# Performance work log

Measured on AMD Instinct MI355X. Metric: run time of the kernel, lower is better.

The kernel has to match this reference:

```python
import jax, jax.numpy as jnp
import numpy as np

B, N, T, IN_DIM, OUT_DIM = 16, 500, 12, 2, 2
H, D, K, NH, NBLOCKS, T_OUT, GDEP = 64, 64, 10, 24, 2, 12, 2
H2 = 2 * H


def setup_inputs():
    key = jax.random.key(0)
    ks = iter(jax.random.split(key, 64))

    def rn(shape, s=1.0):
        return jax.random.normal(next(ks), shape, dtype=jnp.float32) * s

    def z(*shape):
        return jnp.zeros(shape, jnp.float32)

    sI = 1.0 / np.sqrt(IN_DIM)
    sH = 1.0 / np.sqrt(H)
    sH2 = 1.0 / np.sqrt(H2)
    sD = 1.0 / np.sqrt(D)
    adj = jax.random.uniform(next(ks), (N, N), dtype=jnp.float32)
    inp = {
        'x': rn((B, N, T, IN_DIM)),
        'weather': rn((B, T, 4)),
        'geo_adj': adj / adj.sum(1, keepdims=True),
        'fcx_W': rn((IN_DIM, H), sI), 'fcx_b': z(H),
        'env_cb': rn((K, D)), 'nodes_cb': rn((N, D)),
        'w_v': rn((D, K), sD), 'w_k': rn((D, D), sD), 'w_q': rn((D, D), sD),
        'core_W': rn((H, H * H), sH), 'core_b': z(H * H),
        'tcnN_Win': rn((K, H2, H2), sH2), 'tcnN_bin': z(K, H2),
        'tcnN_Wf': rn((K, NBLOCKS, 2, H2, H2), sH2), 'tcnN_bf': z(K, NBLOCKS, H2),
        'tcnN_Wg': rn((K, NBLOCKS, 2, H2, H2), sH2), 'tcnN_bg': z(K, NBLOCKS, H2),
        'tcnN_Wout': rn((K, H2, H), sH2), 'tcnN_bout': z(K, H),
        'tcnP_Win': rn((K, H2, H2), sH2), 'tcnP_bin': z(K, H2),
        'tcnP_Wf': rn((K, NBLOCKS, 2, H2, H2), sH2), 'tcnP_bf': z(K, NBLOCKS, H2),
        'tcnP_Wg': rn((K, NBLOCKS, 2, H2, H2), sH2), 'tcnP_bg': z(K, NBLOCKS, H2),
        'tcnP_Wout': rn((K, H2, H), sH2), 'tcnP_bout': z(K, H),
        'bn1_g': jnp.ones((H,), jnp.float32), 'bn1_b': z(H),
        'bnP_g': jnp.ones((H,), jnp.float32), 'bnP_b': z(H),
        'gcn1_W': rn((H, H), sH), 'gcn1_b': z(H),
        'gcn2_W': rn((H, H), sH), 'gcn2_b': z(H),
        'gcnp_W': rn((H, H), sH), 'gcnp_b': z(H),
        'nv_p1': rn((2 * NH, H)), 'nv_p2': rn((N, H)), 'nv_p3': rn((N, H)),
        'nv_pk': rn((H, H, H), sH),
        'out_W1': rn((T_OUT, H, 100), sH), 'out_b1': z(T_OUT, 100),
        'out_W2': rn((T_OUT, 100, OUT_DIM), 0.1), 'out_b2': z(T_OUT, OUT_DIM),
        't_pos': jax.random.randint(next(ks), (B, T, 2), 0, 7),
        'ind': jax.random.randint(next(ks), (B, T, 2), 0, 7),
    }
    return inp


def _tstep_emb(t, dim):
    half = dim // 2
    freqs = jnp.exp(-jnp.log(10000.0) * jnp.arange(half, dtype=jnp.float32) / half)
    a = t.astype(jnp.float32)[:, None] * freqs[None]
    return jnp.concatenate([jnp.cos(a), jnp.sin(a)], -1)


def _conv2(h, W, b, d):
    # causal kernel-2 dilated conv over time: h [B,N,T,C], W [2,C,Co] -> [B,N,T-d,Co]
    return (jnp.einsum('bntc,co->bnto', h[:, :, :-d], W[0])
            + jnp.einsum('bntc,co->bnto', h[:, :, d:], W[1]) + b)


def _tcn(xin, Win, bin_, Wf, bf, Wg, bg, Wout, bout):
    # gated dilated TCN (Graph-WaveNet style), per node over time
    h = jnp.einsum('bntc,co->bnto', xin, Win) + bin_
    for l in range(Wf.shape[0]):
        d = 2 ** l
        f = jnp.tanh(_conv2(h, Wf[l], bf[l], d))
        g = jax.nn.sigmoid(_conv2(h, Wg[l], bg[l], d))
        h = f * g + h[:, :, d:, :]
    return jnp.einsum('bntc,ch->bnth', h, Wout) + bout


def _bn(h, g, b):
    # BatchNorm1d over channels, stats over (batch, nodes); training mode
    mu = h.mean((0, 1))
    var = h.var((0, 1))
    return g * (h - mu) * jax.lax.rsqrt(var + 1e-5) + b


def _gcn(h, adj, W, b):
    # multi-hop diffusion: sum_{k=0..GDEP} A^k h, then linear
    eq = 'nm,bmh->bnh' if adj.ndim == 2 else 'bnm,bmh->bnh'
    acc, zt = h, h
    for _ in range(GDEP):
        zt = jnp.einsum(eq, adj, zt)
        acc = acc + zt
    return jnp.einsum('bnh,ho->bno', acc, W) + b


def _forward(x, weather, geo_adj, fcx_W, fcx_b, env_cb, nodes_cb, w_v, w_k, w_q,
             core_W, core_b,
             tcnN_Win, tcnN_bin, tcnN_Wf, tcnN_bf, tcnN_Wg, tcnN_bg, tcnN_Wout, tcnN_bout,
             tcnP_Win, tcnP_bin, tcnP_Wf, tcnP_bf, tcnP_Wg, tcnP_bg, tcnP_Wout, tcnP_bout,
             bn1_g, bn1_b, bnP_g, bnP_b, gcn1_W, gcn1_b, gcn2_W, gcn2_b, gcnp_W, gcnp_b,
             nv_p1, nv_p2, nv_p3, nv_pk, out_W1, out_b1, out_W2, out_b2, t_pos, ind):
    scale = 1.0 / jnp.sqrt(jnp.float32(D))
    ind_p = jnp.where(ind[:, :, 0] <= 4, ind[:, :, 1], NH - 1 + ind[:, :, 1])
    tp = jnp.where(t_pos[:, :, 0] <= 4, t_pos[:, :, 1], NH - 1 + t_pos[:, :, 1])
    t_emb = _tstep_emb(tp.reshape(-1), H).reshape(B, T, H)

    # codebook attention -> hard cluster assignment (gumbel softmax, straight-through)
    mat_v = env_cb @ w_v
    mat_k = env_cb @ w_k
    mat_q = nodes_cb @ w_q
    scores = jax.nn.softmax((mat_q @ mat_k.T) * scale, axis=1)
    logits = scores @ mat_v                                   # [N,K]
    gn = jax.random.gumbel(jax.random.key(42), logits.shape, dtype=logits.dtype)
    y_soft = jax.nn.softmax(logits + gn, axis=1)
    hard = jax.nn.one_hot(jnp.argmax(y_soft, axis=1), K, dtype=y_soft.dtype)
    mask = y_soft + jax.lax.stop_gradient(hard - y_soft)      # [N,K] one-hot fwd

    x_emb = jnp.einsum('bnti,ih->bnth', x, fcx_W) + fcx_b
    total_x = jnp.concatenate(
        [x_emb, jnp.broadcast_to(t_emb[:, None], (B, N, T, H))], -1)  # [B,N,T,2H]

    unbias = jnp.zeros((B, N, H), total_x.dtype)
    h_prev = jnp.zeros((B, N, H), total_x.dtype)
    for i in range(K):  # small fixed cluster count
        m = mask[:, i]
        xm = total_x * m[None, :, None, None]
        hn = _tcn(xm[:, :, 1:], tcnN_Win[i], tcnN_bin[i], tcnN_Wf[i], tcnN_bf[i],
                  tcnN_Wg[i], tcnN_bg[i], tcnN_Wout[i], tcnN_bout[i])[:, :, 0, :]
        hp = _tcn(xm[:, :, :-1], tcnP_Win[i], tcnP_bin[i], tcnP_Wf[i], tcnP_bf[i],
                  tcnP_Wg[i], tcnP_bg[i], tcnP_Wout[i], tcnP_bout[i])[:, :, 0, :]
        unbias = unbias + m[None, :, None] * hn
        h_prev = h_prev + m[None, :, None] * hp

    unbias = _bn(unbias, bn1_g, bn1_b)
    h_prev = _bn(h_prev, bnP_g, bnP_b)

    h1 = _gcn(h_prev, geo_adj, gcn1_W, gcn1_b)
    core = (t_emb[:, T - 1] @ core_W + core_b).reshape(B, H, H)
    causal = jax.nn.softmax(jnp.einsum('bnh,bhk,bmk->bnm', unbias, core, h_prev), axis=-1)
    h2 = _gcn(unbias, causal, gcn2_W, gcn2_b)

    te = nv_p1[ind_p[:, -(T - 1)]]                            # [B,H]
    adp = jnp.einsum('ai,ijk->ajk', te, nv_pk)
    adp = jnp.einsum('bj,ajk->abk', nv_p2, adp)
    adp = jnp.einsum('ck,abk->abc', nv_p3, adp)
    adp = jax.nn.softmax(jax.nn.relu(adp), axis=2)            # [B,N,N]
    h3 = _gcn(unbias, adp, gcnp_W, gcnp_b)

    cur_h = h1 + h2 + h3
    hmid = jax.nn.elu(jnp.einsum('bnh,thf->bntf', cur_h, out_W1) + out_b1)
    return jnp.einsum('bntf,tfo->bnto', hmid, out_W2) + out_b2  # [B,N,T_OUT,OUT_DIM]


def reference(x, weather, geo_adj, fcx_W, fcx_b, env_cb, nodes_cb, w_v, w_k, w_q,
              core_W, core_b,
              tcnN_Win, tcnN_bin, tcnN_Wf, tcnN_bf, tcnN_Wg, tcnN_bg, tcnN_Wout, tcnN_bout,
              tcnP_Win, tcnP_bin, tcnP_Wf, tcnP_bf, tcnP_Wg, tcnP_bg, tcnP_Wout, tcnP_bout,
              bn1_g, bn1_b, bnP_g, bnP_b, gcn1_W, gcn1_b, gcn2_W, gcn2_b, gcnp_W, gcnp_b,
              nv_p1, nv_p2, nv_p3, nv_pk, out_W1, out_b1, out_W2, out_b2, t_pos, ind):
    return _forward(x, weather, geo_adj, fcx_W, fcx_b, env_cb, nodes_cb, w_v, w_k, w_q,
                    core_W, core_b,
                    tcnN_Win, tcnN_bin, tcnN_Wf, tcnN_bf, tcnN_Wg, tcnN_bg, tcnN_Wout, tcnN_bout,
                    tcnP_Win, tcnP_bin, tcnP_Wf, tcnP_bf, tcnP_Wg, tcnP_bg, tcnP_Wout, tcnP_bout,
                    bn1_g, bn1_b, bnP_g, bnP_b, gcn1_W, gcn1_b, gcn2_W, gcn2_b, gcnp_W, gcnp_b,
                    nv_p1, nv_p2, nv_p3, nv_pk, out_W1, out_b1, out_W2, out_b2, t_pos, ind)
```

## Files before the change

kernel.cpp:

```cpp
#include <hip/hip_runtime.h>
#include <hip/hip_bf16.h>
#include <math.h>

#define B_ 16
#define N_ 500
#define T_ 12
#define K_ 10
#define NROWS (B_*N_)
#define TROWS 6

__device__ __forceinline__ unsigned rotl32(unsigned v, int r){ return (v<<r)|(v>>(32-r)); }

__device__ __forceinline__ void threefry2x32(unsigned k0, unsigned k1,
                                             unsigned c0, unsigned c1,
                                             unsigned &o0, unsigned &o1){
  unsigned ks2 = k0 ^ k1 ^ 0x1BD11BDAu;
  unsigned x0 = c0 + k0, x1 = c1 + k1;
#define TF_R(r) { x0 += x1; x1 = rotl32(x1,(r)); x1 ^= x0; }
  TF_R(13) TF_R(15) TF_R(26) TF_R(6)
  x0 += k1;  x1 += ks2 + 1u;
  TF_R(17) TF_R(29) TF_R(16) TF_R(24)
  x0 += ks2; x1 += k0 + 2u;
  TF_R(13) TF_R(15) TF_R(26) TF_R(6)
  x0 += k0;  x1 += k1 + 3u;
  TF_R(17) TF_R(29) TF_R(16) TF_R(24)
  x0 += k1;  x1 += ks2 + 4u;
  TF_R(13) TF_R(15) TF_R(26) TF_R(6)
  x0 += ks2; x1 += k0 + 5u;
#undef TF_R
  o0 = x0; o1 = x1;
}

__device__ __forceinline__ float gumbel_at(unsigned idx){
  unsigned b0, b1;
  threefry2x32(0u, 42u, 0u, idx, b0, b1);
  unsigned bits = b0 ^ b1;
  float u = __uint_as_float((bits >> 9) | 0x3f800000u) - 1.0f;
  u = fmaxf(u, 1.17549435e-38f);
  return -logf(-logf(u));
}

__global__ __launch_bounds__(256) void k_matq(const float* __restrict__ nodes_cb,
                                              const float* __restrict__ w_q,
                                              float* __restrict__ matq){
  int idx = blockIdx.x*256 + threadIdx.x;
  if (idx >= N_*64) return;
  int n = idx >> 6, d = idx & 63;
  float a = 0.f;
  for (int c = 0; c < 64; ++c) a += nodes_cb[n*64+c] * w_q[c*64+d];
  matq[idx] = a;
}

__global__ __launch_bounds__(256) void k_route(const float* __restrict__ env_cb,
                                               const float* __restrict__ w_v,
                                               const float* __restrict__ w_k,
                                               const float* __restrict__ matq,
                                               int* __restrict__ node_list,
                                               int* __restrict__ off){
  __shared__ float smk[K_*64];
  __shared__ float smv[K_*K_];
  __shared__ int sroute[N_];
  int tid = threadIdx.x;
  for (int idx = tid; idx < K_*64; idx += 256){
    int kk = idx >> 6, d = idx & 63;
    float a = 0.f;
    for (int c = 0; c < 64; ++c) a += env_cb[kk*64+c] * w_k[c*64+d];
    smk[idx] = a;
  }
  for (int idx = tid; idx < K_*K_; idx += 256){
    int kk = idx / K_, j = idx % K_;
    float a = 0.f;
    for (int c = 0; c < 64; ++c) a += env_cb[kk*64+c] * w_v[c*K_+j];
    smv[idx] = a;
  }
  __syncthreads();
  for (int n = tid; n < N_; n += 256){
    float s[K_];
    float mx = -1e30f;
    for (int j = 0; j < K_; ++j){
      float a = 0.f;
      for (int d = 0; d < 64; ++d) a += matq[n*64+d]*smk[j*64+d];
      s[j] = a * 0.125f;
      mx = fmaxf(mx, s[j]);
    }
    float sum = 0.f;
    for (int j = 0; j < K_; ++j){ s[j] = expf(s[j]-mx); sum += s[j]; }
    float inv = 1.f/sum;
    int best = 0; float bestv = -1e30f;
    for (int j2 = 0; j2 < K_; ++j2){
      float lg = 0.f;
      for (int j = 0; j < K_; ++j) lg += s[j]*inv*smv[j*K_+j2];
      float tot = lg + gumbel_at((unsigned)(n*K_+j2));
      if (tot > bestv){ bestv = tot; best = j2; }
    }
    sroute[n] = best;
  }
  __syncthreads();
  if (tid == 0){
    int cnt[K_]; for (int j=0;j<K_;++j) cnt[j]=0;
    for (int n=0;n<N_;++n) cnt[sroute[n]]++;
    int acc=0;
    for (int j=0;j<K_;++j){ off[j]=acc; acc+=cnt[j]; }
    off[K_]=acc;
    int pos[K_]; for (int j=0;j<K_;++j) pos[j]=off[j];
    for (int n=0;n<N_;++n) node_list[pos[sroute[n]]++] = n;
  }
}

__global__ void k_temb(const int* __restrict__ t_pos, float* __restrict__ temb){
  int tid = threadIdx.x;
  if (tid >= B_*T_) return;
  int b = tid / T_, t = tid % T_;
  int p0 = t_pos[(b*T_+t)*2+0], p1 = t_pos[(b*T_+t)*2+1];
  float tp = (float)((p0 <= 4) ? p1 : 23 + p1);
  float c0 = -logf(10000.f)/32.f;
  for (int j = 0; j < 32; ++j){
    float a = tp * expf(c0 * (float)j);
    temb[(b*T_+t)*64 + j]      = cosf(a);
    temb[(b*T_+t)*64 + 32 + j] = sinf(a);
  }
}

__global__ __launch_bounds__(256) void k_core(const float* __restrict__ temb,
                                              const float* __restrict__ core_W,
                                              const float* __restrict__ core_b,
                                              float* __restrict__ core_f){
  int idx = blockIdx.x*256 + threadIdx.x;
  if (idx >= B_*4096) return;
  int b = idx >> 12, c = idx & 4095;
  const float* te = temb + (b*T_ + 11)*64;
  float a = core_b[c];
  for (int h = 0; h < 64; ++h) a += te[h] * core_W[h*4096 + c];
  core_f[idx] = a;
}

__global__ __launch_bounds__(256) void k_tmp1(const int* __restrict__ ind,
                                              const float* __restrict__ nv_p1,
                                              const float* __restrict__ nv_pk,
                                              float* __restrict__ tmp1){
  int idx = blockIdx.x*256 + threadIdx.x;
  if (idx >= B_*4096) return;
  int b = idx >> 12, c = idx & 4095;
  int i0 = ind[(b*T_+1)*2+0], i1 = ind[(b*T_+1)*2+1];
  int row = (i0 <= 4) ? i1 : 23 + i1;
  const float* te = nv_p1 + row*64;
  float a = 0.f;
  for (int h = 0; h < 64; ++h) a += te[h] * nv_pk[h*4096 + c];
  tmp1[idx] = a;
}

__global__ __launch_bounds__(128) void k_tprep(
    const float* __restrict__ temb,
    const float* __restrict__ fcx_W, const float* __restrict__ fcx_b,
    const float* __restrict__ WinN, const float* __restrict__ WinP,
    float* __restrict__ TE)
{
  int slot = blockIdx.x;
  int y = blockIdx.y;
  int k = slot >> 1, path = slot & 1;
  const float* Win = (path ? WinP : WinN) + k*16384;
  int o = threadIdx.x;
  if (y < 80){
    __shared__ float ste[64];
    int b = y/5, t = y%5;
    if (o < 64) ste[o] = temb[(b*T_ + t)*64 + o];
    __syncthreads();
    float acc = 0.f;
    for (int cc = 0; cc < 64; ++cc) acc += ste[cc] * Win[(64+cc)*128 + o];
    TE[slot*10240 + y*128 + o] = acc;
  } else {
    float a0=0.f, a1=0.f, c0=0.f;
    for (int c = 0; c < 64; ++c){
      float w = Win[c*128 + o];
      a0 += fcx_W[c]*w; a1 += fcx_W[64+c]*w; c0 += fcx_b[c]*w;
    }
    float* AAs = TE + 20*10240 + slot*384;
    AAs[o] = a0; AAs[128+o] = a1; AAs[256+o] = c0;
  }
}

__global__ __launch_bounds__(256) void k_tcn2(
    const float* __restrict__ x,
    const float* __restrict__ TE,
    const int* __restrict__ node_list, const int* __restrict__ off,
    const float* __restrict__ binN,
    const float* __restrict__ WfN,  const float* __restrict__ bfN,
    const float* __restrict__ WgN,  const float* __restrict__ bgN,
    const float* __restrict__ WoutN,const float* __restrict__ boutN,
    const float* __restrict__ binP,
    const float* __restrict__ WfP,  const float* __restrict__ bfP,
    const float* __restrict__ WgP,  const float* __restrict__ bgP,
    const float* __restrict__ WoutP,const float* __restrict__ boutP,
    float* __restrict__ out_unb, float* __restrict__ out_hpr)
{
  int slot = blockIdx.x;
  int k = slot >> 1;
  int path = slot & 1;
  int cnt = off[k+1] - off[k];
  int rows = cnt * 16;
  int r0 = blockIdx.y * TROWS;
  if (r0 >= rows) return;

  const float* bin  = (path ? binP  : binN)  + k*128;
  const float* Wf   = (path ? WfP   : WfN)   + k*4*16384;
  const float* bf_  = (path ? bfP   : bfN)   + k*2*128;
  const float* Wg   = (path ? WgP   : WgN)   + k*4*16384;
  const float* bg_  = (path ? bgP   : bgN)   + k*2*128;
  const float* Wout = (path ? WoutP : WoutN) + k*8192;
  const float* bout = (path ? boutP : boutN) + k*64;
  float* outb = path ? out_hpr : out_unb;
  int t0 = path ? 0 : 1;

  __shared__ __align__(16) float sH0[TROWS*512];
  __shared__ __align__(16) float sH1[TROWS*256];
  __shared__ __align__(16) float sH2[TROWS*128];
  __shared__ float xs[TROWS][4][2];
  __shared__ int rowBN[TROWS];
  __shared__ int rowB[TROWS];

  int tid = threadIdx.x;
  if (tid < TROWS){
    int r = r0 + tid;
    if (r < rows){
      int node = node_list[off[k] + (r >> 4)];
      int b = r & 15;
      rowBN[tid] = b*N_ + node;
      rowB[tid]  = b;
    } else { rowBN[tid] = -1; rowB[tid] = 0; }
  }
  __syncthreads();
  if (tid < TROWS*4){
    int i = tid >> 2, tl = tid & 3;
    int rb = rowBN[i];
    float x0 = 0.f, x1 = 0.f;
    if (rb >= 0){
      const float* xp = x + (rb*T_ + tl + t0)*2;
      x0 = xp[0]; x1 = xp[1];
    }
    xs[i][tl][0] = x0; xs[i][tl][1] = x1;
  }
  __syncthreads();

  {
    int o = tid & 127, half = tid >> 7;
    const float* AAs = TE + 20*10240 + slot*384;
    const float* TEs = TE + slot*10240;
    float a0 = AAs[o], a1 = AAs[128+o], c0 = AAs[256+o];
    float bn = bin[o];
    #pragma unroll
    for (int jj = 0; jj < 12; ++jj){
      int rt = half*12 + jj;
      int i = rt >> 2, tl = rt & 3;
      float v = xs[i][tl][0]*a0 + xs[i][tl][1]*a1 + c0
              + TEs[(rowB[i]*5 + tl + t0)*128 + o] + bn;
      sH0[rt*128 + o] = v;
    }
  }
  __syncthreads();

  {
    int o = tid & 127;
    int jg = (tid >> 7)*6;
    float af[6], ag[6];
    #pragma unroll
    for (int j=0;j<6;++j){ af[j]=0.f; ag[j]=0.f; }
    for (int c = 0; c < 128; c += 4){
      float f00=Wf[(c+0)*128+o], f01=Wf[(c+1)*128+o], f02=Wf[(c+2)*128+o], f03=Wf[(c+3)*128+o];
      float f10=Wf[16384+(c+0)*128+o], f11=Wf[16384+(c+1)*128+o], f12=Wf[16384+(c+2)*128+o], f13=Wf[16384+(c+3)*128+o];
      float g00=Wg[(c+0)*128+o], g01=Wg[(c+1)*128+o], g02=Wg[(c+2)*128+o], g03=Wg[(c+3)*128+o];
      float g10=Wg[16384+(c+0)*128+o], g11=Wg[16384+(c+1)*128+o], g12=Wg[16384+(c+2)*128+o], g13=Wg[16384+(c+3)*128+o];
      #pragma unroll
      for (int jj=0;jj<6;++jj){
        int j = jg + jj;
        int i = j >> 1, ti = j & 1;
        float4 xa = *(const float4*)&sH0[(i*4+ti*2  )*128 + c];
        float4 xb = *(const float4*)&sH0[(i*4+ti*2+1)*128 + c];
        af[jj] += xa.x*f00 + xa.y*f01 + xa.z*f02 + xa.w*f03
                + xb.x*f10 + xb.y*f11 + xb.z*f12 + xb.w*f13;
        ag[jj] += xa.x*g00 + xa.y*g01 + xa.z*g02 + xa.w*g03
                + xb.x*g10 + xb.y*g11 + xb.z*g12 + xb.w*g13;
      }
    }
    float bfv = bf_[o], bgv = bg_[o];
    #pragma unroll
    for (int jj=0;jj<6;++jj){
      int j = jg + jj;
      int i = j >> 1, ti = j & 1;
      float f = tanhf(af[jj] + bfv);
      float g = 1.f/(1.f + expf(-(ag[jj] + bgv)));
      sH1[j*128 + o] = f*g + sH0[(i*4 + ti*2 + 1)*128 + o];
    }
  }
  __syncthreads();

  {
    int o = tid & 127;
    int ig = (tid >> 7)*3;
    const float* Wf1 = Wf + 2*16384;
    const float* Wg1 = Wg + 2*16384;
    float af[3], ag[3];
    #pragma unroll
    for (int i=0;i<3;++i){ af[i]=0.f; ag[i]=0.f; }
    for (int c = 0; c < 128; c += 4){
      float f00=Wf1[(c+0)*128+o], f01=Wf1[(c+1)*128+o], f02=Wf1[(c+2)*128+o], f03=Wf1[(c+3)*128+o];
      float f10=Wf1[16384+(c+0)*128+o], f11=Wf1[16384+(c+1)*128+o], f12=Wf1[16384+(c+2)*128+o], f13=Wf1[16384+(c+3)*128+o];
      float g00=Wg1[(c+0)*128+o], g01=Wg1[(c+1)*128+o], g02=Wg1[(c+2)*128+o], g03=Wg1[(c+3)*128+o];
      float g10=Wg1[16384+(c+0)*128+o], g11=Wg1[16384+(c+1)*128+o], g12=Wg1[16384+(c+2)*128+o], g13=Wg1[16384+(c+3)*128+o];
      #pragma unroll
      for (int ii=0;ii<3;++ii){
        int i = ig + ii;
        float4 xa = *(const float4*)&sH1[(i*2+0)*128 + c];
        float4 xb = *(const float4*)&sH1[(i*2+1)*128 + c];
        af[ii] += xa.x*f00 + xa.y*f01 + xa.z*f02 + xa.w*f03
                + xb.x*f10 + xb.y*f11 + xb.z*f12 + xb.w*f13;
        ag[ii] += xa.x*g00 + xa.y*g01 + xa.z*g02 + xa.w*g03
                + xb.x*g10 + xb.y*g11 + xb.z*g12 + xb.w*g13;
      }
    }
    float bfv = bf_[128+o], bgv = bg_[128+o];
    #pragma unroll
    for (int ii=0;ii<3;++ii){
      int i = ig + ii;
      float f = tanhf(af[ii] + bfv);
      float g = 1.f/(1.f + expf(-(ag[ii] + bgv)));
      sH2[i*128 + o] = f*g + sH1[(i*2+1)*128 + o];
    }
  }
  __syncthreads();

  {
    int o6 = tid & 63, grp = tid >> 6;
    #pragma unroll
    for (int ii=0; ii<2; ++ii){
      int i = grp*2 + ii;
      if (i >= TROWS) continue;
      float acc = 0.f;
      for (int c = 0; c < 128; c += 4){
        float w0=Wout[(c+0)*64+o6], w1=Wout[(c+1)*64+o6],
              w2=Wout[(c+2)*64+o6], w3=Wout[(c+3)*64+o6];
        float4 xv = *(const float4*)&sH2[i*128 + c];
        acc += xv.x*w0 + xv.y*w1 + xv.z*w2 + xv.w*w3;
      }
      if (rowBN[i] >= 0) outb[rowBN[i]*64 + o6] = acc + bout[o6];
    }
  }
}

__global__ __launch_bounds__(256) void k_tcn(
    const float* __restrict__ x,
    const float* __restrict__ fcx_W, const float* __restrict__ fcx_b,
    const float* __restrict__ temb,
    const int* __restrict__ node_list, const int* __restrict__ off,
    const float* __restrict__ WinN, const float* __restrict__ binN,
    const float* __restrict__ WfN,  const float* __restrict__ bfN,
    const float* __restrict__ WgN,  const float* __restrict__ bgN,
    const float* __restrict__ WoutN,const float* __restrict__ boutN,
    const float* __restrict__ WinP, const float* __restrict__ binP,
    const float* __restrict__ WfP,  const float* __restrict__ bfP,
    const float* __restrict__ WgP,  const float* __restrict__ bgP,
    const float* __restrict__ WoutP,const float* __restrict__ boutP,
    float* __restrict__ out_unb, float* __restrict__ out_hpr)
{
  int slot = blockIdx.x;
  int k = slot >> 1;
  int path = slot & 1;
  int cnt = off[k+1] - off[k];
  int rows = cnt * 16;
  int r0 = blockIdx.y * TROWS;
  if (r0 >= rows) return;

  const float* Win  = (path ? WinP  : WinN)  + k*16384;
  const float* bin  = (path ? binP  : binN)  + k*128;
  const float* Wf   = (path ? WfP   : WfN)   + k*4*16384;
  const float* bf_  = (path ? bfP   : bfN)   + k*2*128;
  const float* Wg   = (path ? WgP   : WgN)   + k*4*16384;
  const float* bg_  = (path ? bgP   : bgN)   + k*2*128;
  const float* Wout = (path ? WoutP : WoutN) + k*8192;
  const float* bout = (path ? boutP : boutN) + k*64;
  float* outb = path ? out_hpr : out_unb;
  int t0 = path ? 0 : 1;

  __shared__ __align__(16) float sIn[TROWS*512];
  __shared__ __align__(16) float sH0[TROWS*512];
  __shared__ __align__(16) float sH1[TROWS*256];
  __shared__ __align__(16) float sH2[TROWS*128];
  __shared__ int rowBN[TROWS];
  __shared__ int rowB[TROWS];

  int tid = threadIdx.x;
  if (tid < TROWS){
    int r = r0 + tid;
    if (r < rows){
      int node = node_list[off[k] + (r >> 4)];
      int b = r & 15;
      rowBN[tid] = b*N_ + node;
      rowB[tid]  = b;
    } else { rowBN[tid] = -1; rowB[tid] = 0; }
  }
  __syncthreads();

  for (int i = 0; i < TROWS; ++i){
    int rb = rowBN[i], b = rowB[i];
    for (int c2 = tid; c2 < 512; c2 += 256){
      int t = (c2 >> 7) + t0, c = c2 & 127;
      float v = 0.f;
      if (rb >= 0){
        if (c < 64){
          const float* xp = x + (rb*T_ + t)*2;
          v = xp[0]*fcx_W[c] + xp[1]*fcx_W[64+c] + fcx_b[c];
        } else {
          v = temb[(b*T_ + t)*64 + (c-64)];
        }
      }
      sIn[i*512 + c2] = v;
    }
  }
  __syncthreads();

  {
    int oc = (tid & 63)*2;
    int jg = (tid >> 6)*6;
    float a0[6], a1[6];
    #pragma unroll
    for (int j=0;j<6;++j){ a0[j]=0.f; a1[j]=0.f; }
    for (int c = 0; c < 128; c += 4){
      float2 w0 = *(const float2*)(Win + (c+0)*128 + oc);
      float2 w1 = *(const float2*)(Win + (c+1)*128 + oc);
      float2 w2 = *(const float2*)(Win + (c+2)*128 + oc);
      float2 w3 = *(const float2*)(Win + (c+3)*128 + oc);
      #pragma unroll
      for (int j=0;j<6;++j){
        float4 xv = *(const float4*)&sIn[(jg+j)*128 + c];
        a0[j] += xv.x*w0.x + xv.y*w1.x + xv.z*w2.x + xv.w*w3.x;
        a1[j] += xv.x*w0.y + xv.y*w1.y + xv.z*w2.y + xv.w*w3.y;
      }
    }
    float b0v = bin[oc], b1v = bin[oc+1];
    #pragma unroll
    for (int j=0;j<6;++j){
      sH0[(jg+j)*128 + oc]   = a0[j] + b0v;
      sH0[(jg+j)*128 + oc+1] = a1[j] + b1v;
    }
  }
  __syncthreads();

  {
    int o = tid & 127;
    int jg = (tid >> 7)*6;
    float af[6], ag[6];
    #pragma unroll
    for (int j=0;j<6;++j){ af[j]=0.f; ag[j]=0.f; }
    for (int c = 0; c < 128; c += 4){
      float f00=Wf[(c+0)*128+o], f01=Wf[(c+1)*128+o], f02=Wf[(c+2)*128+o], f03=Wf[(c+3)*128+o];
      float f10=Wf[16384+(c+0)*128+o], f11=Wf[16384+(c+1)*128+o], f12=Wf[16384+(c+2)*128+o], f13=Wf[16384+(c+3)*128+o];
      float g00=Wg[(c+0)*128+o], g01=Wg[(c+1)*128+o], g02=Wg[(c+2)*128+o], g03=Wg[(c+3)*128+o];
      float g10=Wg[16384+(c+0)*128+o], g11=Wg[16384+(c+1)*128+o], g12=Wg[16384+(c+2)*128+o], g13=Wg[16384+(c+3)*128+o];
      #pragma unroll
      for (int jj=0;jj<6;++jj){
        int j = jg + jj;
        int i = j >> 1, ti = j & 1;
        float4 xa = *(const float4*)&sH0[(i*4+ti*2  )*128 + c];
        float4 xb = *(const float4*)&sH0[(i*4+ti*2+1)*128 + c];
        af[jj] += xa.x*f00 + xa.y*f01 + xa.z*f02 + xa.w*f03
                + xb.x*f10 + xb.y*f11 + xb.z*f12 + xb.w*f13;
        ag[jj] += xa.x*g00 + xa.y*g01 + xa.z*g02 + xa.w*g03
                + xb.x*g10 + xb.y*g11 + xb.z*g12 + xb.w*g13;
      }
    }
    float bfv = bf_[o], bgv = bg_[o];
    #pragma unroll
    for (int jj=0;jj<6;++jj){
      int j = jg + jj;
      int i = j >> 1, ti = j & 1;
      float f = tanhf(af[jj] + bfv);
      float g = 1.f/(1.f + expf(-(ag[jj] + bgv)));
      sH1[j*128 + o] = f*g + sH0[(i*4 + ti*2 + 1)*128 + o];
    }
  }
  __syncthreads();

  {
    int o = tid & 127;
    int ig = (tid >> 7)*3;
    const float* Wf1 = Wf + 2*16384;
    const float* Wg1 = Wg + 2*16384;
    float af[3], ag[3];
    #pragma unroll
    for (int i=0;i<3;++i){ af[i]=0.f; ag[i]=0.f; }
    for (int c = 0; c < 128; c += 4){
      float f00=Wf1[(c+0)*128+o], f01=Wf1[(c+1)*128+o], f02=Wf1[(c+2)*128+o], f03=Wf1[(c+3)*128+o];
      float f10=Wf1[16384+(c+0)*128+o], f11=Wf1[16384+(c+1)*128+o], f12=Wf1[16384+(c+2)*128+o], f13=Wf1[16384+(c+3)*128+o];
      float g00=Wg1[(c+0)*128+o], g01=Wg1[(c+1)*128+o], g02=Wg1[(c+2)*128+o], g03=Wg1[(c+3)*128+o];
      float g10=Wg1[16384+(c+0)*128+o], g11=Wg1[16384+(c+1)*128+o], g12=Wg1[16384+(c+2)*128+o], g13=Wg1[16384+(c+3)*128+o];
      #pragma unroll
      for (int ii=0;ii<3;++ii){
        int i = ig + ii;
        float4 xa = *(const float4*)&sH1[(i*2+0)*128 + c];
        float4 xb = *(const float4*)&sH1[(i*2+1)*128 + c];
        af[ii] += xa.x*f00 + xa.y*f01 + xa.z*f02 + xa.w*f03
                + xb.x*f10 + xb.y*f11 + xb.z*f12 + xb.w*f13;
        ag[ii] += xa.x*g00 + xa.y*g01 + xa.z*g02 + xa.w*g03
                + xb.x*g10 + xb.y*g11 + xb.z*g12 + xb.w*g13;
      }
    }
    float bfv = bf_[128+o], bgv = bg_[128+o];
    #pragma unroll
    for (int ii=0;ii<3;++ii){
      int i = ig + ii;
      float f = tanhf(af[ii] + bfv);
      float g = 1.f/(1.f + expf(-(ag[ii] + bgv)));
      sH2[i*128 + o] = f*g + sH1[(i*2+1)*128 + o];
    }
  }
  __syncthreads();

  {
    int o6 = tid & 63, grp = tid >> 6;
    #pragma unroll
    for (int ii=0; ii<2; ++ii){
      int i = grp*2 + ii;
      if (i >= TROWS) continue;
      float acc = 0.f;
      for (int c = 0; c < 128; c += 4){
        float w0=Wout[(c+0)*64+o6], w1=Wout[(c+1)*64+o6],
              w2=Wout[(c+2)*64+o6], w3=Wout[(c+3)*64+o6];
        float4 xv = *(const float4*)&sH2[i*128 + c];
        acc += xv.x*w0 + xv.y*w1 + xv.z*w2 + xv.w*w3;
      }
      if (rowBN[i] >= 0) outb[rowBN[i]*64 + o6] = acc + bout[o6];
    }
  }
}

__global__ __launch_bounds__(256) void k_bnstats(const float* __restrict__ unb,
                                                 const float* __restrict__ hpr,
                                                 float* __restrict__ stats){
  int bid = blockIdx.x;
  int tensor = bid >> 6, c = bid & 63;
  const float* buf = tensor ? hpr : unb;
  float s1 = 0.f, s2 = 0.f;
  for (int r = threadIdx.x; r < NROWS; r += 256){
    float v = buf[r*64 + c];
    s1 += v; s2 += v*v;
  }
  __shared__ float r1[256], r2[256];
  r1[threadIdx.x]=s1; r2[threadIdx.x]=s2;
  __syncthreads();
  for (int s=128; s>0; s>>=1){
    if (threadIdx.x < s){ r1[threadIdx.x]+=r1[threadIdx.x+s]; r2[threadIdx.x]+=r2[threadIdx.x+s]; }
    __syncthreads();
  }
  if (threadIdx.x==0){
    float mean = r1[0]/(float)NROWS;
    float var  = r2[0]/(float)NROWS - mean*mean;
    stats[tensor*128 + c]      = mean;
    stats[tensor*128 + 64 + c] = rsqrtf(var + 1e-5f);
  }
}

__global__ __launch_bounds__(256) void k_bnapply(float* __restrict__ unb, float* __restrict__ hpr,
                                                 const float* __restrict__ stats,
                                                 const float* __restrict__ g1, const float* __restrict__ be1,
                                                 const float* __restrict__ gP, const float* __restrict__ beP){
  int idx = blockIdx.x*256 + threadIdx.x;
  if (idx >= 2*NROWS*64) return;
  int tensor = idx >= NROWS*64;
  int local = idx - tensor*NROWS*64;
  int c = local & 63;
  float* buf = tensor ? hpr : unb;
  float mean = stats[tensor*128+c], rstd = stats[tensor*128+64+c];
  float g = tensor ? gP[c] : g1[c];
  float bb = tensor ? beP[c] : be1[c];
  buf[local] = g * (buf[local]-mean) * rstd + bb;
}

template<int AMODE, int RELU, int FINAL, int ADD>
__global__ __launch_bounds__(256) void k_attn(
    const float* __restrict__ geo,
    const float* __restrict__ Qf, const float* __restrict__ Qb,
    const float* __restrict__ M,
    const float* __restrict__ Keysf, const float* __restrict__ Keysb,
    const float* __restrict__ X,
    const float* __restrict__ X0, const float* __restrict__ Z1,
    const float* __restrict__ Wg, const float* __restrict__ bg,
    float* __restrict__ cur, float* __restrict__ Y)
{
  __shared__ __align__(16) float kbuf[64][65];
  __shared__ __align__(16) float xbuf[64][64];
  __shared__ __align__(16) float vbuf[16][64];
  __shared__ __align__(16) float pbuf[16][64];

  int b = blockIdx.y, n0 = blockIdx.x*16;
  int tid = threadIdx.x;
  int nl = tid >> 5, ml = tid & 31;
  int nA = n0 + nl, nB = n0 + nl + 8;
  float rrK[16], rrX[16], rrA[4];

  if (AMODE != 0){
    for (int idx = tid; idx < 1024; idx += 256){
      int r = idx >> 6, kk = idx & 63;
      int nn = n0 + r;
      float q = 0.f;
      if (nn < N_) q = (AMODE == 1) ? Qf[(b*N_+nn)*64+kk] : Qb[nn*64+kk];
      pbuf[r][kk] = q;
    }
    for (int idx = tid; idx < 4096; idx += 256)
      kbuf[idx>>6][idx&63] = M[b*4096 + idx];
    __syncthreads();
    float vxA = 0.f, vyA = 0.f, vxB = 0.f, vyB = 0.f;
    for (int kk = 0; kk < 64; ++kk){
      float qA = pbuf[nl][kk], qB = pbuf[nl+8][kk];
      float2 m2 = *(const float2*)&kbuf[kk][ml*2];
      vxA += qA*m2.x; vyA += qA*m2.y;
      vxB += qB*m2.x; vyB += qB*m2.y;
    }
    __syncthreads();
    vbuf[nl  ][ml*2] = vxA; vbuf[nl  ][ml*2+1] = vyA;
    vbuf[nl+8][ml*2] = vxB; vbuf[nl+8][ml*2+1] = vyB;
  }
  {
    if (AMODE != 0) __syncthreads();
    #pragma unroll
    for (int ii = 0; ii < 16; ++ii){
      int idx = tid + ii*256;
      int mm = idx >> 6, kk = idx & 63;
      if (AMODE != 0)
        kbuf[mm][kk] = (AMODE == 1) ? Keysf[(b*N_+mm)*64+kk] : Keysb[mm*64+kk];
      xbuf[mm][kk] = X[(b*N_+mm)*64+kk];
    }
    if (AMODE == 0){
      #pragma unroll
      for (int ii = 0; ii < 4; ++ii){
        int idx = tid + ii*256;
        int r = idx >> 6, mm = idx & 63;
        int nn = n0 + r;
        pbuf[r][mm] = (nn < N_) ? geo[nn*N_ + mm] : 0.f;
      }
    }
// ... 278 lines not shown
      l_runB = l_runB*scaleB + lcB; m_runB = mnewB;
      accxA *= scaleA; accyA *= scaleA;
      accxB *= scaleB; accyB *= scaleB;
      pbuf[nl  ][ml]    = p0A;
      pbuf[nl  ][ml+32] = p1A;
      pbuf[nl+8][ml]    = p0B;
      pbuf[nl+8][ml+32] = p1B;
    }
    __syncthreads();
    for (int mm = 0; mm < 64; mm += 4){
      float4 pA = *(const float4*)&pbuf[nl  ][mm];
      float4 pB = *(const float4*)&pbuf[nl+8][mm];
      float2 x0 = *(const float2*)&xbuf[mm+0][ml*2];
      float2 x1 = *(const float2*)&xbuf[mm+1][ml*2];
      float2 x2 = *(const float2*)&xbuf[mm+2][ml*2];
      float2 x3 = *(const float2*)&xbuf[mm+3][ml*2];
      accxA += pA.x*x0.x + pA.y*x1.x + pA.z*x2.x + pA.w*x3.x;
      accyA += pA.x*x0.y + pA.y*x1.y + pA.z*x2.y + pA.w*x3.y;
      accxB += pB.x*x0.x + pB.y*x1.x + pB.z*x2.x + pB.w*x3.x;
      accyB += pB.x*x0.y + pB.y*x1.y + pB.z*x2.y + pB.w*x3.y;
    }
    __syncthreads();
    if (ci < 7){
      #pragma unroll
      for (int ii=0; ii<16; ++ii){
        int idx = tid + ii*256;
        kbuf[idx>>6][idx&63] = rrK[ii];
        xbuf[idx>>6][idx&63] = rrX[ii];
      }
      __syncthreads();
    }
  }
  float invA = 1.f / l_runA, invB = 1.f / l_runB;
  accxA *= invA; accyA *= invA;
  accxB *= invB; accyB *= invB;
  if (nA < N_){
    float2 o2; o2.x = accxA; o2.y = accyA;
    *(float2*)&Y[(b*N_+nA)*64 + ml*2] = o2;
  }
  if (nB < N_){
    float2 o2; o2.x = accxB; o2.y = accyB;
    *(float2*)&Y[(b*N_+nB)*64 + ml*2] = o2;
  }
}

template<int ADD>
__global__ __launch_bounds__(256) void k_attn_p2(
    const float* __restrict__ Pb,
    const float* __restrict__ X,
    const float* __restrict__ X0,
    const float* __restrict__ Wg, const float* __restrict__ bg,
    float* __restrict__ cur)
{
  __shared__ __align__(16) float pbuf[16][516];
  __shared__ __align__(16) float xbuf[64][64];
  __shared__ __align__(16) float vbuf[16][64];

  int b = blockIdx.y, n0 = blockIdx.x*16;
  int tid = threadIdx.x;
  int nl = tid >> 5, ml = tid & 31;
  int nA = n0 + nl, nB = n0 + nl + 8;
  float rrX[16];

  for (int idx = tid; idx < 16*512; idx += 256){
    int r = idx >> 9, m = idx & 511;
    int nn = n0 + r;
    pbuf[r][m] = (nn < N_) ? Pb[((long)(b*N_+nn))*512 + m] : -1e30f;
  }
  __syncthreads();
  float lmaxA = -1e30f, lmaxB = -1e30f;
  for (int m = ml; m < 512; m += 32){
    lmaxA = fmaxf(lmaxA, pbuf[nl  ][m]);
    lmaxB = fmaxf(lmaxB, pbuf[nl+8][m]);
  }
  #pragma unroll
  for (int msk=1; msk<32; msk<<=1){
    lmaxA = fmaxf(lmaxA, __shfl_xor(lmaxA, msk, 32));
    lmaxB = fmaxf(lmaxB, __shfl_xor(lmaxB, msk, 32));
  }
  float lsumA = 0.f, lsumB = 0.f;
  for (int m = ml; m < 512; m += 32){
    float pA = expf(pbuf[nl  ][m] - lmaxA);
    float pB = expf(pbuf[nl+8][m] - lmaxB);
    pbuf[nl  ][m] = pA;
    pbuf[nl+8][m] = pB;
    lsumA += pA; lsumB += pB;
  }
  #pragma unroll
  for (int msk=1; msk<32; msk<<=1){
    lsumA += __shfl_xor(lsumA, msk, 32);
    lsumB += __shfl_xor(lsumB, msk, 32);
  }
  float invA = 1.f/lsumA, invB = 1.f/lsumB;
  for (int m = ml; m < 512; m += 32){
    pbuf[nl  ][m] *= invA;
    pbuf[nl+8][m] *= invB;
  }

  #pragma unroll
  for (int ii=0; ii<16; ++ii){
    int idx = tid + ii*256;
    int mm = idx>>6, kk = idx&63;
    xbuf[mm][kk] = X[(b*N_+mm)*64+kk];
  }
  __syncthreads();

  float accxA = 0.f, accyA = 0.f, accxB = 0.f, accyB = 0.f;
  for (int ci = 0; ci < 8; ++ci){
    int m0 = ci*64;
    if (ci < 7){
      #pragma unroll
      for (int ii=0; ii<16; ++ii){
        int idx = tid + ii*256;
        int mm = idx>>6, kk = idx&63;
        int m = m0+64+mm;
        rrX[ii] = (m < N_) ? X[(b*N_+m)*64+kk] : 0.f;
      }
    }
    for (int mm = 0; mm < 64; mm += 4){
      float4 pA = *(const float4*)&pbuf[nl  ][m0+mm];
      float4 pB = *(const float4*)&pbuf[nl+8][m0+mm];
      float2 x0 = *(const float2*)&xbuf[mm+0][ml*2];
      float2 x1 = *(const float2*)&xbuf[mm+1][ml*2];
      float2 x2 = *(const float2*)&xbuf[mm+2][ml*2];
      float2 x3 = *(const float2*)&xbuf[mm+3][ml*2];
      accxA += pA.x*x0.x + pA.y*x1.x + pA.z*x2.x + pA.w*x3.x;
      accyA += pA.x*x0.y + pA.y*x1.y + pA.z*x2.y + pA.w*x3.y;
      accxB += pB.x*x0.x + pB.y*x1.x + pB.z*x2.x + pB.w*x3.x;
      accyB += pB.x*x0.y + pB.y*x1.y + pB.z*x2.y + pB.w*x3.y;
    }
    __syncthreads();
    if (ci < 7){
      #pragma unroll
      for (int ii=0; ii<16; ++ii){
        int idx = tid + ii*256;
        xbuf[idx>>6][idx&63] = rrX[ii];
      }
      __syncthreads();
    }
  }

  {
    float svxA = 0.f, svyA = 0.f, svxB = 0.f, svyB = 0.f;
    if (nA < N_){
      int row = b*N_ + nA;
      float2 x0v = *(const float2*)&X0[row*64 + ml*2];
      float2 z1v = *(const float2*)&X[row*64 + ml*2];
      svxA = accxA + x0v.x + z1v.x;
      svyA = accyA + x0v.y + z1v.y;
    }
    if (nB < N_){
      int row = b*N_ + nB;
      float2 x0v = *(const float2*)&X0[row*64 + ml*2];
      float2 z1v = *(const float2*)&X[row*64 + ml*2];
      svxB = accxB + x0v.x + z1v.x;
      svyB = accyB + x0v.y + z1v.y;
    }
    vbuf[nl  ][ml*2] = svxA; vbuf[nl  ][ml*2+1] = svyA;
    vbuf[nl+8][ml*2] = svxB; vbuf[nl+8][ml*2+1] = svyB;
    for (int idx = tid; idx < 4096; idx += 256)
      xbuf[idx>>6][idx&63] = Wg[idx];
    __syncthreads();
    float oxA = 0.f, oyA = 0.f, oxB = 0.f, oyB = 0.f;
    for (int kk = 0; kk < 64; ++kk){
      float sA = vbuf[nl][kk], sB = vbuf[nl+8][kk];
      float2 w2 = *(const float2*)&xbuf[kk][ml*2];
      oxA += sA*w2.x; oyA += sA*w2.y;
      oxB += sB*w2.x; oyB += sB*w2.y;
    }
    float2 bv = *(const float2*)&bg[ml*2];
    if (nA < N_){
      int row = b*N_ + nA;
      float vx = oxA + bv.x, vy = oyA + bv.y;
      if (ADD){
        float2 old = *(const float2*)&cur[row*64 + ml*2];
        vx += old.x; vy += old.y;
      }
      float2 o2; o2.x = vx; o2.y = vy;
      *(float2*)&cur[row*64 + ml*2] = o2;
    }
    if (nB < N_){
      int row = b*N_ + nB;
      float vx = oxB + bv.x, vy = oyB + bv.y;
      if (ADD){
        float2 old = *(const float2*)&cur[row*64 + ml*2];
        vx += old.x; vy += old.y;
      }
      float2 o2; o2.x = vx; o2.y = vy;
      *(float2*)&cur[row*64 + ml*2] = o2;
    }
  }
}

__global__ __launch_bounds__(128) void k_out(const float* __restrict__ cur,
                                             const float* __restrict__ W1, const float* __restrict__ bb1,
                                             const float* __restrict__ W2, const float* __restrict__ bb2,
                                             float* __restrict__ out){
  __shared__ float ch[4][64];
  __shared__ float hid[4*1200];
  int tid = threadIdx.x;
  int rbase = blockIdx.x*4;
  for (int idx = tid; idx < 256; idx += 128){
    int r = idx >> 6, h = idx & 63;
    ch[r][h] = cur[(rbase+r)*64 + h];
  }
  __syncthreads();
  for (int job = tid; job < 1200; job += 128){
    int t = job / 100, f = job - t*100;
    float a0 = bb1[t*100+f], a1 = a0, a2 = a0, a3 = a0;
    for (int h = 0; h < 64; ++h){
      float w = W1[(t*64+h)*100 + f];
      a0 += ch[0][h]*w; a1 += ch[1][h]*w; a2 += ch[2][h]*w; a3 += ch[3][h]*w;
    }
    hid[0*1200+job] = (a0 > 0.f) ? a0 : expm1f(a0);
    hid[1*1200+job] = (a1 > 0.f) ? a1 : expm1f(a1);
    hid[2*1200+job] = (a2 > 0.f) ? a2 : expm1f(a2);
    hid[3*1200+job] = (a3 > 0.f) ? a3 : expm1f(a3);
  }
  __syncthreads();
  if (tid < 96){
    int r = tid / 24, rem = tid % 24;
    int t = rem >> 1, o = rem & 1;
    float a = bb2[t*2+o];
    const float* hp = hid + r*1200 + t*100;
    for (int f = 0; f < 100; ++f) a += hp[f] * W2[(t*100+f)*2+o];
    out[(rbase+r)*24 + t*2+o] = a;
  }
}

extern "C" void kernel_launch(void* const* d_in, const int* in_sizes, int n_in,
                              void* d_out, int out_size, void* d_ws, size_t ws_size,
                              hipStream_t stream)
{
  const float* x        = (const float*)d_in[0];
  const float* geo      = (const float*)d_in[2];
  const float* fcx_W    = (const float*)d_in[3];
  const float* fcx_b    = (const float*)d_in[4];
  const float* env_cb   = (const float*)d_in[5];
  const float* nodes_cb = (const float*)d_in[6];
  const float* w_v      = (const float*)d_in[7];
  const float* w_k      = (const float*)d_in[8];
  const float* w_q      = (const float*)d_in[9];
  const float* core_W   = (const float*)d_in[10];
  const float* core_b   = (const float*)d_in[11];
  const float* tN_Win   = (const float*)d_in[12];
  const float* tN_bin   = (const float*)d_in[13];
  const float* tN_Wf    = (const float*)d_in[14];
  const float* tN_bf    = (const float*)d_in[15];
  const float* tN_Wg    = (const float*)d_in[16];
  const float* tN_bg    = (const float*)d_in[17];
  const float* tN_Wout  = (const float*)d_in[18];
  const float* tN_bout  = (const float*)d_in[19];
  const float* tP_Win   = (const float*)d_in[20];
  const float* tP_bin   = (const float*)d_in[21];
  const float* tP_Wf    = (const float*)d_in[22];
  const float* tP_bf    = (const float*)d_in[23];
  const float* tP_Wg    = (const float*)d_in[24];
  const float* tP_bg    = (const float*)d_in[25];
  const float* tP_Wout  = (const float*)d_in[26];
  const float* tP_bout  = (const float*)d_in[27];
  const float* bn1_g    = (const float*)d_in[28];
  const float* bn1_b    = (const float*)d_in[29];
  const float* bnP_g    = (const float*)d_in[30];
  const float* bnP_b    = (const float*)d_in[31];
  const float* gcn1_W   = (const float*)d_in[32];
  const float* gcn1_b   = (const float*)d_in[33];
  const float* gcn2_W   = (const float*)d_in[34];
  const float* gcn2_b   = (const float*)d_in[35];
  const float* gcnp_W   = (const float*)d_in[36];
  const float* gcnp_b   = (const float*)d_in[37];
  const float* nv_p1    = (const float*)d_in[38];
  const float* nv_p2    = (const float*)d_in[39];
  const float* nv_p3    = (const float*)d_in[40];
  const float* nv_pk    = (const float*)d_in[41];
  const float* out_W1   = (const float*)d_in[42];
  const float* out_b1   = (const float*)d_in[43];
  const float* out_W2   = (const float*)d_in[44];
  const float* out_b2   = (const float*)d_in[45];
  const int*   t_pos    = (const int*)d_in[46];
  const int*   ind      = (const int*)d_in[47];

  int* node_list = (int*)d_ws;
  int* off       = node_list + 512;
  float* F = (float*)((char*)d_ws + 4096);
  float* temb   = F + 0;
  float* core_f = F + 12288;
  float* tmp1   = F + 77824;
  float* stats  = F + 143360;
  float* matq   = F + 143616;
  float* unb    = F + 175616;
  float* hpr    = F + 687616;
  float* cur    = F + 1199616;
  float* zt1    = F + 1711616;
  float* Pb     = F + 2223616;
  float* TE     = Pb;
  bool useP = ws_size >= (size_t)(4096 + (size_t)(2223616 + 4096000)*4);

  k_matq <<<dim3(125), dim3(256), 0, stream>>>(nodes_cb, w_q, matq);
  k_route<<<dim3(1),   dim3(256), 0, stream>>>(env_cb, w_v, w_k, matq, node_list, off);
  k_temb <<<dim3(1),   dim3(192), 0, stream>>>(t_pos, temb);
  k_core <<<dim3(256), dim3(256), 0, stream>>>(temb, core_W, core_b, core_f);
  if (useP){
    k_tprep<<<dim3(20, 81), dim3(128), 0, stream>>>(temb, fcx_W, fcx_b, tN_Win, tP_Win, TE);
    k_tcn2 <<<dim3(20, 334), dim3(256), 0, stream>>>(x, TE, node_list, off,
        tN_bin, tN_Wf, tN_bf, tN_Wg, tN_bg, tN_Wout, tN_bout,
        tP_bin, tP_Wf, tP_bf, tP_Wg, tP_bg, tP_Wout, tP_bout,
        unb, hpr);
  } else {
    k_tcn  <<<dim3(20, 334), dim3(256), 0, stream>>>(x, fcx_W, fcx_b, temb, node_list, off,
        tN_Win, tN_bin, tN_Wf, tN_bf, tN_Wg, tN_bg, tN_Wout, tN_bout,
        tP_Win, tP_bin, tP_Wf, tP_bf, tP_Wg, tP_bg, tP_Wout, tP_bout,
        unb, hpr);
  }
  k_bnstats<<<dim3(128), dim3(256), 0, stream>>>(unb, hpr, stats);
  k_bnapply<<<dim3(4000),dim3(256), 0, stream>>>(unb, hpr, stats, bn1_g, bn1_b, bnP_g, bnP_b);
  k_tmp1<<<dim3(256), dim3(256), 0, stream>>>(ind, nv_p1, nv_pk, tmp1);

  dim3 ag(32, 16);
  const float* nil = nullptr;
  k_attn<0,0,0,0><<<ag, 256, 0, stream>>>(geo, nil,nil,nil, nil,nil,
                                 hpr, nil,nil, nil,nil, nullptr, zt1);
  k_attn<0,0,1,0><<<ag, 256, 0, stream>>>(geo, nil,nil,nil, nil,nil,
                                 zt1, hpr, zt1, gcn1_W, gcn1_b, cur, nullptr);
  if (useP){
    k_attn_p1<1,0><<<ag, 256, 0, stream>>>(unb, nil, core_f, hpr, nil, unb, Pb, zt1);
    k_attn_p2<1>  <<<ag, 256, 0, stream>>>(Pb, zt1, unb, gcn2_W, gcn2_b, cur);
  } else {
    k_attn<1,0,0,0><<<ag, 256, 0, stream>>>(nil, unb,nil, core_f, hpr,nil,
                                   unb, nil,nil, nil,nil, nullptr, zt1);
    k_attn<1,0,1,1><<<ag, 256, 0, stream>>>(nil, unb,nil, core_f, hpr,nil,
                                   zt1, unb, zt1, gcn2_W, gcn2_b, cur, nullptr);
  }
  if (useP){
    k_attn_p1<2,1><<<ag, 256, 0, stream>>>(nil, nv_p2, tmp1, nil, nv_p3, unb, Pb, zt1);
    k_attn_p2<1>  <<<ag, 256, 0, stream>>>(Pb, zt1, unb, gcnp_W, gcnp_b, cur);
  } else {
    k_attn<2,1,0,0><<<ag, 256, 0, stream>>>(nil, nil,nv_p2, tmp1, nil,nv_p3,
                                   unb, nil,nil, nil,nil, nullptr, zt1);
    k_attn<2,1,1,1><<<ag, 256, 0, stream>>>(nil, nil,nv_p2, tmp1, nil,nv_p3,
                                   zt1, unb, zt1, gcnp_W, gcnp_b, cur, nullptr);
  }
  k_out<<<dim3(2000), dim3(128), 0, stream>>>(cur, out_W1, out_b1, out_W2, out_b2, (float*)d_out);
}
```

Baseline: 927.7 us.

## Double rows per block in tcn2, vectorize weight loads, XCD-aware block mapping

The k_tcn2 kernel now handles 12 rows per block instead of 6, and each thread computes two output channels from float2 weight loads. This halves the number of blocks and doubles how many rows reuse each weight load. The 2D grid becomes a 1D grid with a remap that gives each XCD a contiguous range of work, so blocks sharing the same expert weights land on the same L2. The cost is more registers per thread (four accumulator arrays), which could lower occupancy, plus fewer, larger blocks.

```diff
diff --git a/kernel.cpp b/kernel.cpp
--- a/kernel.cpp
+++ b/kernel.cpp
@@ -8,6 +8,8 @@
 #define K_ 10
 #define NROWS (B_*N_)
 #define TROWS 6
+#define TR2 12
+#define YB2 167
 
 __device__ __forceinline__ unsigned rotl32(unsigned v, int r){ return (v<<r)|(v>>(32-r)); }
 
@@ -193,12 +195,18 @@
     const float* __restrict__ WoutP,const float* __restrict__ boutP,
     float* __restrict__ out_unb, float* __restrict__ out_hpr)
 {
-  int slot = blockIdx.x;
+  const int NW = 20*YB2;
+  int id = blockIdx.x;
+  int qq = NW >> 3, rr = NW & 7;
+  int xcd = id & 7, pos = id >> 3;
+  int work = (xcd < rr) ? xcd*(qq+1) + pos : rr*(qq+1) + (xcd-rr)*qq + pos;
+  int slot = work / YB2;
+  int r0   = (work - slot*YB2) * TR2;
+
   int k = slot >> 1;
   int path = slot & 1;
   int cnt = off[k+1] - off[k];
   int rows = cnt * 16;
-  int r0 = blockIdx.y * TROWS;
   if (r0 >= rows) return;
 
   const float* bin  = (path ? binP  : binN)  + k*128;
@@ -211,15 +219,15 @@
   float* outb = path ? out_hpr : out_unb;
   int t0 = path ? 0 : 1;
 
-  __shared__ __align__(16) float sH0[TROWS*512];
-  __shared__ __align__(16) float sH1[TROWS*256];
-  __shared__ __align__(16) float sH2[TROWS*128];
-  __shared__ float xs[TROWS][4][2];
-  __shared__ int rowBN[TROWS];
-  __shared__ int rowB[TROWS];
+  __shared__ __align__(16) float sH0[TR2*4*128];
+  __shared__ __align__(16) float sH1[TR2*2*128];
+  __shared__ __align__(16) float sH2[TR2*128];
+  __shared__ float xs[TR2][4][2];
+  __shared__ int rowBN[TR2];
+  __shared__ int rowB[TR2];
 
   int tid = threadIdx.x;
-  if (tid < TROWS){
+  if (tid < TR2){
     int r = r0 + tid;
     if (r < rows){
       int node = node_list[off[k] + (r >> 4)];
@@ -229,7 +237,7 @@
     } else { rowBN[tid] = -1; rowB[tid] = 0; }
   }
   __syncthreads();
-  if (tid < TROWS*4){
+  if (tid < TR2*4){
     int i = tid >> 2, tl = tid & 3;
     int rb = rowBN[i];
     float x0 = 0.f, x1 = 0.f;
@@ -248,8 +256,8 @@
     float a0 = AAs[o], a1 = AAs[128+o], c0 = AAs[256+o];
     float bn = bin[o];
     #pragma unroll
-    for (int jj = 0; jj < 12; ++jj){
-      int rt = half*12 + jj;
+    for (int jj = 0; jj < 24; ++jj){
+      int rt = half*24 + jj;
       int i = rt >> 2, tl = rt & 3;
       float v = xs[i][tl][0]*a0 + xs[i][tl][1]*a1 + c0
               + TEs[(rowB[i]*5 + tl + t0)*128 + o] + bn;
@@ -259,71 +267,95 @@
   __syncthreads();
 
   {
-    int o = tid & 127;
-    int jg = (tid >> 7)*6;
-    float af[6], ag[6];
-    #pragma unroll
-    for (int j=0;j<6;++j){ af[j]=0.f; ag[j]=0.f; }
+    int op = (tid & 63)*2;
+    int jg = (tid >> 6)*6;
+    float af0[6], af1[6], ag0[6], ag1[6];
+    #pragma unroll
+    for (int j=0;j<6;++j){ af0[j]=0.f; af1[j]=0.f; ag0[j]=0.f; ag1[j]=0.f; }
     for (int c = 0; c < 128; c += 4){
-      float f00=Wf[(c+0)*128+o], f01=Wf[(c+1)*128+o], f02=Wf[(c+2)*128+o], f03=Wf[(c+3)*128+o];
-      float f10=Wf[16384+(c+0)*128+o], f11=Wf[16384+(c+1)*128+o], f12=Wf[16384+(c+2)*128+o], f13=Wf[16384+(c+3)*128+o];
-      float g00=Wg[(c+0)*128+o], g01=Wg[(c+1)*128+o], g02=Wg[(c+2)*128+o], g03=Wg[(c+3)*128+o];
-      float g10=Wg[16384+(c+0)*128+o], g11=Wg[16384+(c+1)*128+o], g12=Wg[16384+(c+2)*128+o], g13=Wg[16384+(c+3)*128+o];
+      float2 f00=*(const float2*)&Wf[(c+0)*128+op], f01=*(const float2*)&Wf[(c+1)*128+op],
+             f02=*(const float2*)&Wf[(c+2)*128+op], f03=*(const float2*)&Wf[(c+3)*128+op];
+      float2 f10=*(const float2*)&Wf[16384+(c+0)*128+op], f11=*(const float2*)&Wf[16384+(c+1)*128+op],
+             f12=*(const float2*)&Wf[16384+(c+2)*128+op], f13=*(const float2*)&Wf[16384+(c+3)*128+op];
+      float2 g00=*(const float2*)&Wg[(c+0)*128+op], g01=*(const float2*)&Wg[(c+1)*128+op],
+             g02=*(const float2*)&Wg[(c+2)*128+op], g03=*(const float2*)&Wg[(c+3)*128+op];
+      float2 g10=*(const float2*)&Wg[16384+(c+0)*128+op], g11=*(const float2*)&Wg[16384+(c+1)*128+op],
+             g12=*(const float2*)&Wg[16384+(c+2)*128+op], g13=*(const float2*)&Wg[16384+(c+3)*128+op];
       #pragma unroll
       for (int jj=0;jj<6;++jj){
         int j = jg + jj;
         int i = j >> 1, ti = j & 1;
         float4 xa = *(const float4*)&sH0[(i*4+ti*2  )*128 + c];
         float4 xb = *(const float4*)&sH0[(i*4+ti*2+1)*128 + c];
-        af[jj] += xa.x*f00 + xa.y*f01 + xa.z*f02 + xa.w*f03
-                + xb.x*f10 + xb.y*f11 + xb.z*f12 + xb.w*f13;
-        ag[jj] += xa.x*g00 + xa.y*g01 + xa.z*g02 + xa.w*g03
-                + xb.x*g10 + xb.y*g11 + xb.z*g12 + xb.w*g13;
-      }
-    }
-    float bfv = bf_[o], bgv = bg_[o];
+        af0[jj] += xa.x*f00.x + xa.y*f01.x + xa.z*f02.x + xa.w*f03.x
+                 + xb.x*f10.x + xb.y*f11.x + xb.z*f12.x + xb.w*f13.x;
+        af1[jj] += xa.x*f00.y + xa.y*f01.y + xa.z*f02.y + xa.w*f03.y
+                 + xb.x*f10.y + xb.y*f11.y + xb.z*f12.y + xb.w*f13.y;
+        ag0[jj] += xa.x*g00.x + xa.y*g01.x + xa.z*g02.x + xa.w*g03.x
+                 + xb.x*g10.x + xb.y*g11.x + xb.z*g12.x + xb.w*g13.x;
+        ag1[jj] += xa.x*g00.y + xa.y*g01.y + xa.z*g02.y + xa.w*g03.y
+                 + xb.x*g10.y + xb.y*g11.y + xb.z*g12.y + xb.w*g13.y;
+      }
+    }
+    float bfv0 = bf_[op], bfv1 = bf_[op+1], bgv0 = bg_[op], bgv1 = bg_[op+1];
     #pragma unroll
     for (int jj=0;jj<6;++jj){
       int j = jg + jj;
       int i = j >> 1, ti = j & 1;
-      float f = tanhf(af[jj] + bfv);
-      float g = 1.f/(1.f + expf(-(ag[jj] + bgv)));
-      sH1[j*128 + o] = f*g + sH0[(i*4 + ti*2 + 1)*128 + o];
+      float f0 = tanhf(af0[jj] + bfv0);
+      float g0 = 1.f/(1.f + expf(-(ag0[jj] + bgv0)));
+      float f1 = tanhf(af1[jj] + bfv1);
+      float g1 = 1.f/(1.f + expf(-(ag1[jj] + bgv1)));
+      float2 res = *(const float2*)&sH0[(i*4 + ti*2 + 1)*128 + op];
+      float2 o2; o2.x = f0*g0 + res.x; o2.y = f1*g1 + res.y;
+      *(float2*)&sH1[j*128 + op] = o2;
     }
   }
   __syncthreads();
 
   {
-    int o = tid & 127;
-    int ig = (tid >> 7)*3;
+    int op = (tid & 63)*2;
+    int ig = (tid >> 6)*3;
     const float* Wf1 = Wf + 2*16384;
     const float* Wg1 = Wg + 2*16384;
-    float af[3], ag[3];
-    #pragma unroll
-    for (int i=0;i<3;++i){ af[i]=0.f; ag[i]=0.f; }
+    float af0[3], af1[3], ag0[3], ag1[3];
+    #pragma unroll
+    for (int i=0;i<3;++i){ af0[i]=0.f; af1[i]=0.f; ag0[i]=0.f; ag1[i]=0.f; }
     for (int c = 0; c < 128; c += 4){
-      float f00=Wf1[(c+0)*128+o], f01=Wf1[(c+1)*128+o], f02=Wf1[(c+2)*128+o], f03=Wf1[(c+3)*128+o];
-      float f10=Wf1[16384+(c+0)*128+o], f11=Wf1[16384+(c+1)*128+o], f12=Wf1[16384+(c+2)*128+o], f13=Wf1[16384+(c+3)*128+o];
-      float g00=Wg1[(c+0)*128+o], g01=Wg1[(c+1)*128+o], g02=Wg1[(c+2)*128+o], g03=Wg1[(c+3)*128+o];
-      float g10=Wg1[16384+(c+0)*128+o], g11=Wg1[16384+(c+1)*128+o], g12=Wg1[16384+(c+2)*128+o], g13=Wg1[16384+(c+3)*128+o];
+      float2 f00=*(const float2*)&Wf1[(c+0)*128+op], f01=*(const float2*)&Wf1[(c+1)*128+op],
+             f02=*(const float2*)&Wf1[(c+2)*128+op], f03=*(const float2*)&Wf1[(c+3)*128+op];
+      float2 f10=*(const float2*)&Wf1[16384+(c+0)*128+op], f11=*(const float2*)&Wf1[16384+(c+1)*128+op],
+             f12=*(const float2*)&Wf1[16384+(c+2)*128+op], f13=*(const float2*)&Wf1[16384+(c+3)*128+op];
+      float2 g00=*(const float2*)&Wg1[(c+0)*128+op], g01=*(const float2*)&Wg1[(c+1)*128+op],
+             g02=*(const float2*)&Wg1[(c+2)*128+op], g03=*(const float2*)&Wg1[(c+3)*128+op];
+      float2 g10=*(const float2*)&Wg1[16384+(c+0)*128+op], g11=*(const float2*)&Wg1[16384+(c+1)*128+op],
+             g12=*(const float2*)&Wg1[16384+(c+2)*128+op], g13=*(const float2*)&Wg1[16384+(c+3)*128+op];
       #pragma unroll
       for (int ii=0;ii<3;++ii){
         int i = ig + ii;
         float4 xa = *(const float4*)&sH1[(i*2+0)*128 + c];
         float4 xb = *(const float4*)&sH1[(i*2+1)*128 + c];
-        af[ii] += xa.x*f00 + xa.y*f01 + xa.z*f02 + xa.w*f03
-                + xb.x*f10 + xb.y*f11 + xb.z*f12 + xb.w*f13;
-        ag[ii] += xa.x*g00 + xa.y*g01 + xa.z*g02 + xa.w*g03
-                + xb.x*g10 + xb.y*g11 + xb.z*g12 + xb.w*g13;
-      }
-    }
-    float bfv = bf_[128+o], bgv = bg_[128+o];
+        af0[ii] += xa.x*f00.x + xa.y*f01.x + xa.z*f02.x + xa.w*f03.x
+                 + xb.x*f10.x + xb.y*f11.x + xb.z*f12.x + xb.w*f13.x;
+        af1[ii] += xa.x*f00.y + xa.y*f01.y + xa.z*f02.y + xa.w*f03.y
+                 + xb.x*f10.y + xb.y*f11.y + xb.z*f12.y + xb.w*f13.y;
+        ag0[ii] += xa.x*g00.x + xa.y*g01.x + xa.z*g02.x + xa.w*g03.x
+                 + xb.x*g10.x + xb.y*g11.x + xb.z*g12.x + xb.w*g13.x;
+        ag1[ii] += xa.x*g00.y + xa.y*g01.y + xa.z*g02.y + xa.w*g03.y
+                 + xb.x*g10.y + xb.y*g11.y + xb.z*g12.y + xb.w*g13.y;
+      }
+    }
+    float bfv0 = bf_[128+op], bfv1 = bf_[128+op+1], bgv0 = bg_[128+op], bgv1 = bg_[128+op+1];
     #pragma unroll
     for (int ii=0;ii<3;++ii){
       int i = ig + ii;
-      float f = tanhf(af[ii] + bfv);
-      float g = 1.f/(1.f + expf(-(ag[ii] + bgv)));
-      sH2[i*128 + o] = f*g + sH1[(i*2+1)*128 + o];
+      float f0 = tanhf(af0[ii] + bfv0);
+      float g0 = 1.f/(1.f + expf(-(ag0[ii] + bgv0)));
+      float f1 = tanhf(af1[ii] + bfv1);
+      float g1 = 1.f/(1.f + expf(-(ag1[ii] + bgv1)));
+      float2 res = *(const float2*)&sH1[(i*2+1)*128 + op];
+      float2 o2; o2.x = f0*g0 + res.x; o2.y = f1*g1 + res.y;
+      *(float2*)&sH2[i*128 + op] = o2;
     }
   }
   __syncthreads();
@@ -331,9 +363,8 @@
   {
     int o6 = tid & 63, grp = tid >> 6;
     #pragma unroll
-    for (int ii=0; ii<2; ++ii){
-      int i = grp*2 + ii;
-      if (i >= TROWS) continue;
+    for (int ii=0; ii<3; ++ii){
+      int i = grp*3 + ii;
       float acc = 0.f;
       for (int c = 0; c < 128; c += 4){
         float w0=Wout[(c+0)*64+o6], w1=Wout[(c+1)*64+o6],
@@ -1218,7 +1249,7 @@
   k_core <<<dim3(256), dim3(256), 0, stream>>>(temb, core_W, core_b, core_f);
   if (useP){
     k_tprep<<<dim3(20, 81), dim3(128), 0, stream>>>(temb, fcx_W, fcx_b, tN_Win, tP_Win, TE);
-    k_tcn2 <<<dim3(20, 334), dim3(256), 0, stream>>>(x, TE, node_list, off,
+    k_tcn2 <<<dim3(20*YB2), dim3(256), 0, stream>>>(x, TE, node_list, off,
         tN_bin, tN_Wf, tN_bf, tN_Wg, tN_bg, tN_Wout, tN_bout,
         tP_bin, tP_Wf, tP_bf, tP_Wg, tP_bg, tP_Wout, tP_bout,
         unb, hpr);
```

Result: slower. 1.169 ms (+26.0%).
